# Optimization experiments

Hardware: AMD Instinct MI355X
Metric: run time of the kernel (lower is better)

The kernel has to match this reference:

```python
import jax, jax.numpy as jnp
import numpy as np

N = 1_000_000
D_IN = 64
D_HID = 128
NUM_SEG = 8192


def setup_inputs() -> dict:
    key = jax.random.key(0)
    ks = jax.random.split(key, 8)
    f_all = jax.random.normal(ks[0], (N, D_IN), dtype=jnp.float32)
    seg_ids = jnp.sort(jax.random.randint(ks[1], (N,), 0, NUM_SEG, dtype=jnp.int32))
    W1 = jax.random.normal(ks[2], (D_IN, 32), dtype=jnp.float32) * 0.1
    b1 = jax.random.normal(ks[3], (32,), dtype=jnp.float32) * 0.1
    W2 = jax.random.normal(ks[4], (32, 64), dtype=jnp.float32) * 0.1
    b2 = jax.random.normal(ks[5], (64,), dtype=jnp.float32) * 0.1
    W3 = jax.random.normal(ks[6], (64, D_HID), dtype=jnp.float32) * 0.1
    b3 = jax.random.normal(ks[7], (D_HID,), dtype=jnp.float32) * 0.1
    return {"f_all": f_all, "seg_ids": seg_ids, "num_segments": NUM_SEG,
            "W1": W1, "b1": b1, "W2": W2, "b2": b2, "W3": W3, "b3": b3}


def reference(f_all, seg_ids, num_segments, W1, b1, W2, b2, W3, b3):
    # 3-layer MLP: input -> 32 -> 64 -> hidden_size, ReLU on first two
    y = jax.nn.relu(f_all @ W1 + b1)          # [N, 32]
    y = jax.nn.relu(y @ W2 + b2)              # [N, 64]
    y = y @ W3 + b3                           # [N, hidden]
    # per-segment mean; empty segments stay zero (matches torch.zeros init)
    sums = jax.ops.segment_sum(y, seg_ids, num_segments=num_segments)           # [S, hidden]
    counts = jax.ops.segment_sum(jnp.ones((f_all.shape[0],), y.dtype), seg_ids,
                                 num_segments=num_segments)                     # [S]
    return sums / jnp.maximum(counts, 1.0)[:, None]
```

## Files before the change

### kernel.cpp

```cpp
#include <hip/hip_runtime.h>

constexpr int D_IN  = 64;
constexpr int D_H1  = 32;
constexpr int D_H2  = 64;
constexpr int D_OUT = 128;
constexpr int NSEG  = 8192;

constexpr int BLOCK = 256;
constexpr int RT    = 64;
constexpr int TPB   = 8;

typedef __bf16 bfx8 __attribute__((ext_vector_type(8)));
typedef __bf16 bfx4 __attribute__((ext_vector_type(4)));
typedef float  fx4  __attribute__((ext_vector_type(4)));


#define BAR_LGKM() do {                                        \
    asm volatile("s_waitcnt lgkmcnt(0)" ::: "memory");         \
    __builtin_amdgcn_s_barrier();                              \
    __builtin_amdgcn_sched_barrier(0);                         \
} while (0)

__global__ __launch_bounds__(BLOCK, 3) void mlp_seg_mfma(
    const float* __restrict__ f, const int* __restrict__ seg,
    const float* __restrict__ W1, const float* __restrict__ b1,
    const float* __restrict__ W2, const float* __restrict__ b2,
    const float* __restrict__ W3, const float* __restrict__ b3,
    float* __restrict__ sums, float* __restrict__ counts,
    int N, int ntiles)
{
    __shared__ __align__(16) __bf16 sf [RT * 64];
    __shared__ __align__(16) __bf16 sh1[RT * 32];
    __shared__ __align__(16) __bf16 sh2[RT * 64];
    __shared__ __align__(16) __bf16 syT[D_OUT * 64];
    __shared__ int sseg[2][RT];

    const int tid  = threadIdx.x;
    const int wv   = tid >> 6;
    const int lane = tid & 63;
    const int lr   = lane & 15;
    const int quad = lane >> 4;
    const int m0   = wv * 16;
    const int ar   = m0 + lr;

    bfx8 fw1[2][2];
    #pragma unroll
    for (int j = 0; j < 2; ++j)
        #pragma unroll
        for (int ks = 0; ks < 2; ++ks)
            #pragma unroll
            for (int i = 0; i < 8; ++i)
                fw1[j][ks][i] = (__bf16)W1[(ks*32 + quad*8 + i)*D_H1 + j*16 + lr];

    bfx8 fw2[4];
    #pragma unroll
    for (int j = 0; j < 4; ++j)
        #pragma unroll
        for (int i = 0; i < 8; ++i)
            fw2[j][i] = (__bf16)W2[(quad*8 + i)*D_H2 + j*16 + lr];

    bfx8 fw3[2][2];
    #pragma unroll
    for (int j = 0; j < 2; ++j)
        #pragma unroll
        for (int ks = 0; ks < 2; ++ks)
            #pragma unroll
            for (int i = 0; i < 8; ++i)
                fw3[j][ks][i] = (__bf16)W3[(ks*32 + quad*8 + i)*D_OUT + wv*32 + j*16 + lr];

    fx4 rb1v[2], rb2v[4];
    #pragma unroll
    for (int j = 0; j < 2; ++j)
        #pragma unroll
        for (int rg = 0; rg < 4; ++rg) rb1v[j][rg] = b1[j*16 + quad*4 + rg];
    #pragma unroll
    for (int j = 0; j < 4; ++j)
        #pragma unroll
        for (int rg = 0; rg < 4; ++rg) rb2v[j][rg] = b2[j*16 + quad*4 + rg];
    float rb3[2];
    #pragma unroll
    for (int j = 0; j < 2; ++j) rb3[j] = b3[wv*32 + j*16 + lr];

    const int colA = tid & 127;
    const int grp  = tid >> 7;
    int   cur_seg = -1;
    float run_sum = 0.f;
    int   run_len = 0;

    const int t0 = blockIdx.x * TPB;
    const int t1 = min(t0 + TPB, ntiles);

    {
        const int R0 = t0 * RT;
        const float4* f4 = (const float4*)f + (size_t)R0 * 16;
        #pragma unroll
        for (int i = 0; i < 4; ++i) {
            const int idx4 = tid + i * 256;
            float4 qq = make_float4(0.f, 0.f, 0.f, 0.f);
            if ((size_t)R0 * 64 + (size_t)idx4 * 4 < (size_t)N * 64) qq = f4[idx4];
            const int r = idx4 >> 4;
            const int c = (idx4 & 15) * 4;
            bfx4 v;
            v[0] = (__bf16)qq.x; v[1] = (__bf16)qq.y;
            v[2] = (__bf16)qq.z; v[3] = (__bf16)qq.w;
            *(bfx4*)&sf[r*64 + (((c >> 3) ^ (r & 7)) << 3) + (c & 7)] = v;
        }
        if (tid < RT) sseg[0][tid] = (R0 + tid < N) ? seg[R0 + tid] : -2;
    }
    __syncthreads();

    int p = 0;
    for (int t = t0; t < t1; ++t, p ^= 1) {
        const int R0 = t * RT;
        const bool havenext = (t + 1 < t1);

        float4 q[4];
        int rseg = -2;
        if (havenext) {
            const float4* f4n = (const float4*)f + (size_t)(R0 + RT) * 16;
            #pragma unroll
            for (int i = 0; i < 4; ++i) {
                const int idx4 = tid + i * 256;
                q[i] = make_float4(0.f, 0.f, 0.f, 0.f);
                if ((size_t)(R0 + RT) * 64 + (size_t)idx4 * 4 < (size_t)N * 64)
                    q[i] = f4n[idx4];
            }
            if (tid < RT) rseg = (R0 + RT + tid < N) ? seg[R0 + RT + tid] : -2;
        }

        fx4 acc1[2] = {{0,0,0,0},{0,0,0,0}};
        #pragma unroll
        for (int ks = 0; ks < 2; ++ks) {
            bfx8 a = *(const bfx8*)&sf[ar*64 + (((ks*4 + quad) ^ (ar & 7)) << 3)];
            #pragma unroll
            for (int j = 0; j < 2; ++j)
                acc1[j] = __builtin_amdgcn_mfma_f32_16x16x32_bf16(fw1[j][ks], a, acc1[j], 0, 0, 0);
        }
        #pragma unroll
        for (int j = 0; j < 2; ++j) {
            bfx4 w;
            #pragma unroll
            for (int rg = 0; rg < 4; ++rg)
                w[rg] = (__bf16)fmaxf(acc1[j][rg] + rb1v[j][rg], 0.f);
            const int b = j*2 + (quad >> 1);
            *(bfx4*)&sh1[ar*32 + ((b ^ (ar & 3)) << 3) + (quad & 1)*4] = w;
        }

        fx4 acc2[4] = {{0,0,0,0},{0,0,0,0},{0,0,0,0},{0,0,0,0}};
        {
            bfx8 a = *(const bfx8*)&sh1[ar*32 + ((quad ^ (ar & 3)) << 3)];
            #pragma unroll
            for (int j = 0; j < 4; ++j)
                acc2[j] = __builtin_amdgcn_mfma_f32_16x16x32_bf16(fw2[j], a, acc2[j], 0, 0, 0);
        }
        #pragma unroll
        for (int j = 0; j < 4; ++j) {
            bfx4 w;
            #pragma unroll
            for (int rg = 0; rg < 4; ++rg)
                w[rg] = (__bf16)fmaxf(acc2[j][rg] + rb2v[j][rg], 0.f);
            const int b = j*2 + (quad >> 1);
            *(bfx4*)&sh2[ar*64 + ((b ^ (ar & 7)) << 3) + (quad & 1)*4] = w;
        }

        BAR_LGKM();

        #pragma unroll
        for (int mt = 0; mt < 4; ++mt) {
            fx4 acc3[2] = {{0,0,0,0},{0,0,0,0}};
            const int arow = mt*16 + lr;
            #pragma unroll
            for (int ks = 0; ks < 2; ++ks) {
                bfx8 a = *(const bfx8*)&sh2[arow*64 + (((ks*4 + quad) ^ (arow & 7)) << 3)];
                #pragma unroll
                for (int j = 0; j < 2; ++j)
                    acc3[j] = __builtin_amdgcn_mfma_f32_16x16x32_bf16(a, fw3[j][ks], acc3[j], 0, 0, 0);
            }
            #pragma unroll
            for (int j = 0; j < 2; ++j) {
                bfx4 w;
                #pragma unroll
                for (int rg = 0; rg < 4; ++rg)
                    w[rg] = (__bf16)(acc3[j][rg] + rb3[j]);
                const int col  = wv*32 + j*16 + lr;
                const int row0 = mt*16 + quad*4;
                *(bfx4*)&syT[col*64 + (((row0 >> 3) ^ (col & 7)) << 3) + (quad & 1)*4] = w;
            }
        }

        if (havenext) {
            #pragma unroll
            for (int i = 0; i < 4; ++i) {
                const int idx4 = tid + i * 256;
                const int r = idx4 >> 4;
                const int c = (idx4 & 15) * 4;
                bfx4 v;
                v[0] = (__bf16)q[i].x; v[1] = (__bf16)q[i].y;
                v[2] = (__bf16)q[i].z; v[3] = (__bf16)q[i].w;
                *(bfx4*)&sf[r*64 + (((c >> 3) ^ (r & 7)) << 3) + (c & 7)] = v;
            }
            if (tid < RT) sseg[p ^ 1][tid] = rseg;
        }

        BAR_LGKM();

        #pragma unroll
        for (int ch = 0; ch < 4; ++ch) {
            const int r8 = grp*32 + ch*8;
            const bfx8 v8 = *(const bfx8*)&syT[colA*64 + (((grp*4 + ch) ^ (colA & 7)) << 3)];
            const int sA = sseg[p][r8];
            const int sB = sseg[p][r8 + 7];
            if (sA == sB) {
                float sum = 0.f;
                #pragma unroll
                for (int k = 0; k < 8; ++k) sum += (float)v8[k];
                if (sA != cur_seg) {
                    if (cur_seg >= 0) {
                        atomicAdd(&sums[(size_t)cur_seg * D_OUT + colA], run_sum);
                        if (colA == 0) atomicAdd(&counts[cur_seg], (float)run_len);
                    }
                    cur_seg = sA; run_sum = sum; run_len = 8;
                } else {
                    run_sum += sum; run_len += 8;
                }
            } else {
                #pragma unroll
                for (int k = 0; k < 8; ++k) {
                    const int s = sseg[p][r8 + k];
                    if (s != cur_seg) {
                        if (cur_seg >= 0) {
                            atomicAdd(&sums[(size_t)cur_seg * D_OUT + colA], run_sum);
                            if (colA == 0) atomicAdd(&counts[cur_seg], (float)run_len);
                        }
                        cur_seg = s; run_sum = 0.f; run_len = 0;
                    }
                    run_sum += (float)v8[k]; run_len++;
                }
            }
        }
    }

    if (cur_seg >= 0) {
        atomicAdd(&sums[(size_t)cur_seg * D_OUT + colA], run_sum);
        if (colA == 0) atomicAdd(&counts[cur_seg], (float)run_len);
    }
}

__global__ __launch_bounds__(256) void div_kernel(
    const float* __restrict__ sums, const float* __restrict__ counts,
    float* __restrict__ out, int total)
{
    const int i = blockIdx.x * 256 + threadIdx.x;
    if (i < total) out[i] = sums[i] / fmaxf(counts[i >> 7], 1.f);
}

extern "C" void kernel_launch(void* const* d_in, const int* in_sizes, int n_in,
                              void* d_out, int out_size, void* d_ws, size_t ws_size,
                              hipStream_t stream) {
    const float* f   = (const float*)d_in[0];
    const int*   seg = (const int*)  d_in[1];
    const float* W1 = (const float*)d_in[3];
    const float* b1 = (const float*)d_in[4];
    const float* W2 = (const float*)d_in[5];
    const float* b2 = (const float*)d_in[6];
    const float* W3 = (const float*)d_in[7];
    const float* b3 = (const float*)d_in[8];
    float* out = (float*)d_out;

    const int N = in_sizes[0] / D_IN;

    float* sums   = (float*)d_ws;
    float* counts = sums + (size_t)NSEG * D_OUT;

    hipMemsetAsync(d_ws, 0, ((size_t)NSEG * D_OUT + NSEG) * sizeof(float), stream);

    const int ntiles  = (N + RT - 1) / RT;
    const int nblocks = (ntiles + TPB - 1) / TPB;
    mlp_seg_mfma<<<nblocks, BLOCK, 0, stream>>>(f, seg, W1, b1, W2, b2, W3, b3,
                                                sums, counts, N, ntiles);

    const int total = NSEG * D_OUT;
    div_kernel<<<(total + 255) / 256, 256, 0, stream>>>(sums, counts, out, total);
}
```

Before: 403.9 us.

## Reduce layer-3 MFMA outputs directly in registers and use persistent block partition

Removes the transposed syT staging buffer and reduces the layer-3 MFMA accumulators straight into per-lane running segment sums, folding the bias in as count times b3 at flush time. The feature and hidden-2 buffers are double-buffered and segment ids go into a triple buffer, which removes one block barrier per tile. The launch changes from fixed 8-tile blocks to a persistent grid of 768 blocks, each taking a contiguous range of tiles, so there are fewer segment-boundary atomic flushes. The cost is more live accumulator registers per lane. Each lane also now walks rows serially, with divergent branches wherever a segment boundary falls inside its rows.

```diff
diff --git a/kernel.cpp b/kernel.cpp
--- a/kernel.cpp
+++ b/kernel.cpp
@@ -8,7 +8,7 @@
 
 constexpr int BLOCK = 256;
 constexpr int RT    = 64;
-constexpr int TPB   = 8;
+constexpr int NB    = 768;
 
 typedef __bf16 bfx8 __attribute__((ext_vector_type(8)));
 typedef __bf16 bfx4 __attribute__((ext_vector_type(4)));
@@ -29,11 +29,10 @@
     float* __restrict__ sums, float* __restrict__ counts,
     int N, int ntiles)
 {
-    __shared__ __align__(16) __bf16 sf [RT * 64];
+    __shared__ __align__(16) __bf16 sf [2][RT * 64];
     __shared__ __align__(16) __bf16 sh1[RT * 32];
-    __shared__ __align__(16) __bf16 sh2[RT * 64];
-    __shared__ __align__(16) __bf16 syT[D_OUT * 64];
-    __shared__ int sseg[2][RT];
+    __shared__ __align__(16) __bf16 sh2[2][RT * 64];
+    __shared__ __align__(16) int sseg3[3][RT];
 
     const int tid  = threadIdx.x;
     const int wv   = tid >> 6;
@@ -81,17 +80,20 @@
     #pragma unroll
     for (int j = 0; j < 2; ++j) rb3[j] = b3[wv*32 + j*16 + lr];
 
-    const int colA = tid & 127;
-    const int grp  = tid >> 7;
+    const int  col0    = wv*32 + lr;
+    const bool cntlane = (wv == 0) && (lr == 0);
     int   cur_seg = -1;
-    float run_sum = 0.f;
-    int   run_len = 0;
-
-    const int t0 = blockIdx.x * TPB;
-    const int t1 = min(t0 + TPB, ntiles);
-
-    {
-        const int R0 = t0 * RT;
+    float rs0 = 0.f, rs1 = 0.f;
+    int   rlen = 0;
+
+    const int nb   = gridDim.x;
+    const int bb   = blockIdx.x;
+    const int base = ntiles / nb, rem = ntiles % nb;
+    const int tstart = bb * base + min(bb, rem);
+    const int cnt    = base + (bb < rem ? 1 : 0);
+
+    if (cnt > 0) {
+        const int R0 = tstart * RT;
         const float4* f4 = (const float4*)f + (size_t)R0 * 16;
         #pragma unroll
         for (int i = 0; i < 4; ++i) {
@@ -103,35 +105,38 @@
             bfx4 v;
             v[0] = (__bf16)qq.x; v[1] = (__bf16)qq.y;
             v[2] = (__bf16)qq.z; v[3] = (__bf16)qq.w;
-            *(bfx4*)&sf[r*64 + (((c >> 3) ^ (r & 7)) << 3) + (c & 7)] = v;
-        }
-        if (tid < RT) sseg[0][tid] = (R0 + tid < N) ? seg[R0 + tid] : -2;
+            *(bfx4*)&sf[0][r*64 + (((c >> 3) ^ (r & 7)) << 3) + (c & 7)] = v;
+        }
+        if (tid < RT) sseg3[0][tid] = (R0 + tid < N) ? seg[R0 + tid] : -2;
     }
     __syncthreads();
 
-    int p = 0;
-    for (int t = t0; t < t1; ++t, p ^= 1) {
-        const int R0 = t * RT;
-        const bool havenext = (t + 1 < t1);
+    int p3 = 0;
+    for (int i = 0; i < cnt; ++i) {
+        const int t  = tstart + i;
+        const int p2 = i & 1;
+        const int p3n = (p3 + 1 == 3) ? 0 : p3 + 1;
+        const bool havenext = (i + 1 < cnt);
 
         float4 q[4];
         int rseg = -2;
         if (havenext) {
-            const float4* f4n = (const float4*)f + (size_t)(R0 + RT) * 16;
-            #pragma unroll
-            for (int i = 0; i < 4; ++i) {
-                const int idx4 = tid + i * 256;
-                q[i] = make_float4(0.f, 0.f, 0.f, 0.f);
-                if ((size_t)(R0 + RT) * 64 + (size_t)idx4 * 4 < (size_t)N * 64)
-                    q[i] = f4n[idx4];
-            }
-            if (tid < RT) rseg = (R0 + RT + tid < N) ? seg[R0 + RT + tid] : -2;
+            const int Rn = (t + 1) * RT;
+            const float4* f4n = (const float4*)f + (size_t)Rn * 16;
+            #pragma unroll
+            for (int k = 0; k < 4; ++k) {
+                const int idx4 = tid + k * 256;
+                q[k] = make_float4(0.f, 0.f, 0.f, 0.f);
+                if ((size_t)Rn * 64 + (size_t)idx4 * 4 < (size_t)N * 64)
+                    q[k] = f4n[idx4];
+            }
+            if (tid < RT) rseg = (Rn + tid < N) ? seg[Rn + tid] : -2;
         }
 
         fx4 acc1[2] = {{0,0,0,0},{0,0,0,0}};
         #pragma unroll
         for (int ks = 0; ks < 2; ++ks) {
-            bfx8 a = *(const bfx8*)&sf[ar*64 + (((ks*4 + quad) ^ (ar & 7)) << 3)];
+            bfx8 a = *(const bfx8*)&sf[p2][ar*64 + (((ks*4 + quad) ^ (ar & 7)) << 3)];
             #pragma unroll
             for (int j = 0; j < 2; ++j)
                 acc1[j] = __builtin_amdgcn_mfma_f32_16x16x32_bf16(fw1[j][ks], a, acc1[j], 0, 0, 0);
@@ -160,89 +165,67 @@
             for (int rg = 0; rg < 4; ++rg)
                 w[rg] = (__bf16)fmaxf(acc2[j][rg] + rb2v[j][rg], 0.f);
             const int b = j*2 + (quad >> 1);
-            *(bfx4*)&sh2[ar*64 + ((b ^ (ar & 7)) << 3) + (quad & 1)*4] = w;
-        }
-
-        BAR_LGKM();
-
-        #pragma unroll
-        for (int mt = 0; mt < 4; ++mt) {
-            fx4 acc3[2] = {{0,0,0,0},{0,0,0,0}};
-            const int arow = mt*16 + lr;
-            #pragma unroll
-            for (int ks = 0; ks < 2; ++ks) {
-                bfx8 a = *(const bfx8*)&sh2[arow*64 + (((ks*4 + quad) ^ (arow & 7)) << 3)];
-                #pragma unroll
-                for (int j = 0; j < 2; ++j)
-                    acc3[j] = __builtin_amdgcn_mfma_f32_16x16x32_bf16(a, fw3[j][ks], acc3[j], 0, 0, 0);
-            }
-            #pragma unroll
-            for (int j = 0; j < 2; ++j) {
-                bfx4 w;
-                #pragma unroll
-                for (int rg = 0; rg < 4; ++rg)
-                    w[rg] = (__bf16)(acc3[j][rg] + rb3[j]);
-                const int col  = wv*32 + j*16 + lr;
-                const int row0 = mt*16 + quad*4;
-                *(bfx4*)&syT[col*64 + (((row0 >> 3) ^ (col & 7)) << 3) + (quad & 1)*4] = w;
-            }
+            *(bfx4*)&sh2[p2][ar*64 + ((b ^ (ar & 7)) << 3) + (quad & 1)*4] = w;
         }
 
         if (havenext) {
             #pragma unroll
-            for (int i = 0; i < 4; ++i) {
-                const int idx4 = tid + i * 256;
+            for (int k = 0; k < 4; ++k) {
+                const int idx4 = tid + k * 256;
                 const int r = idx4 >> 4;
                 const int c = (idx4 & 15) * 4;
                 bfx4 v;
-                v[0] = (__bf16)q[i].x; v[1] = (__bf16)q[i].y;
-                v[2] = (__bf16)q[i].z; v[3] = (__bf16)q[i].w;
-                *(bfx4*)&sf[r*64 + (((c >> 3) ^ (r & 7)) << 3) + (c & 7)] = v;
-            }
-            if (tid < RT) sseg[p ^ 1][tid] = rseg;
+                v[0] = (__bf16)q[k].x; v[1] = (__bf16)q[k].y;
+                v[2] = (__bf16)q[k].z; v[3] = (__bf16)q[k].w;
+                *(bfx4*)&sf[p2 ^ 1][r*64 + (((c >> 3) ^ (r & 7)) << 3) + (c & 7)] = v;
+            }
+            if (tid < RT) sseg3[p3n][tid] = rseg;
         }
 
         BAR_LGKM();
 
-        #pragma unroll
-        for (int ch = 0; ch < 4; ++ch) {
-            const int r8 = grp*32 + ch*8;
-            const bfx8 v8 = *(const bfx8*)&syT[colA*64 + (((grp*4 + ch) ^ (colA & 7)) << 3)];
-            const int sA = sseg[p][r8];
-            const int sB = sseg[p][r8 + 7];
-            if (sA == sB) {
-                float sum = 0.f;
+        fx4 acc3[4][2];
+        #pragma unroll
+        for (int mt = 0; mt < 4; ++mt) {
+            acc3[mt][0] = (fx4){0,0,0,0};
+            acc3[mt][1] = (fx4){0,0,0,0};
+            const int arow = mt*16 + lr;
+            #pragma unroll
+            for (int ks = 0; ks < 2; ++ks) {
+                bfx8 a = *(const bfx8*)&sh2[p2][arow*64 + (((ks*4 + quad) ^ (arow & 7)) << 3)];
                 #pragma unroll
-                for (int k = 0; k < 8; ++k) sum += (float)v8[k];
-                if (sA != cur_seg) {
+                for (int j = 0; j < 2; ++j)
+                    acc3[mt][j] = __builtin_amdgcn_mfma_f32_16x16x32_bf16(a, fw3[j][ks], acc3[mt][j], 0, 0, 0);
+            }
+        }
+
+        #pragma unroll
+        for (int mt = 0; mt < 4; ++mt) {
+            const int4 s4 = *(const int4*)&sseg3[p3][mt*16 + quad*4];
+            const int ss[4] = {s4.x, s4.y, s4.z, s4.w};
+            #pragma unroll
+            for (int rg = 0; rg < 4; ++rg) {
+                const int s = ss[rg];
+                if (s != cur_seg) {
                     if (cur_seg >= 0) {
-                        atomicAdd(&sums[(size_t)cur_seg * D_OUT + colA], run_sum);
-                        if (colA == 0) atomicAdd(&counts[cur_seg], (float)run_len);
+                        atomicAdd(&sums[(size_t)cur_seg * D_OUT + col0],      rs0 + (float)rlen * rb3[0]);
+                        atomicAdd(&sums[(size_t)cur_seg * D_OUT + col0 + 16], rs1 + (float)rlen * rb3[1]);
+                        if (cntlane) atomicAdd(&counts[cur_seg], (float)rlen);
                     }
-                    cur_seg = sA; run_sum = sum; run_len = 8;
-                } else {
-                    run_sum += sum; run_len += 8;
+                    cur_seg = s; rs0 = 0.f; rs1 = 0.f; rlen = 0;
                 }
-            } else {
-                #pragma unroll
-                for (int k = 0; k < 8; ++k) {
-                    const int s = sseg[p][r8 + k];
-                    if (s != cur_seg) {
-                        if (cur_seg >= 0) {
-                            atomicAdd(&sums[(size_t)cur_seg * D_OUT + colA], run_sum);
-                            if (colA == 0) atomicAdd(&counts[cur_seg], (float)run_len);
-                        }
-                        cur_seg = s; run_sum = 0.f; run_len = 0;
-                    }
-                    run_sum += (float)v8[k]; run_len++;
-                }
-            }
-        }
+                rs0 += acc3[mt][0][rg];
+                rs1 += acc3[mt][1][rg];
+                ++rlen;
+            }
+        }
+        p3 = p3n;
     }
 
     if (cur_seg >= 0) {
-        atomicAdd(&sums[(size_t)cur_seg * D_OUT + colA], run_sum);
-        if (colA == 0) atomicAdd(&counts[cur_seg], (float)run_len);
+        atomicAdd(&sums[(size_t)cur_seg * D_OUT + col0],      rs0 + (float)rlen * rb3[0]);
+        atomicAdd(&sums[(size_t)cur_seg * D_OUT + col0 + 16], rs1 + (float)rlen * rb3[1]);
+        if (cntlane) atomicAdd(&counts[cur_seg], (float)rlen);
     }
 }
 
@@ -275,7 +258,7 @@
     hipMemsetAsync(d_ws, 0, ((size_t)NSEG * D_OUT + NSEG) * sizeof(float), stream);
 
     const int ntiles  = (N + RT - 1) / RT;
-    const int nblocks = (ntiles + TPB - 1) / TPB;
+    const int nblocks = min(NB, ntiles);
     mlp_seg_mfma<<<nblocks, BLOCK, 0, stream>>>(f, seg, W1, b1, W2, b2, W3, b3,
                                                 sums, counts, N, ntiles);
 
```

Result: slower. 415.3 us (+2.8%).
